# Kernel tuning notes

Measured on AMD Instinct MI355X. Metric: run time of the kernel, lower is better.

The kernel has to match this reference:

```python
import jax, jax.numpy as jnp
import numpy as np
import math

BLOCK_SIZE = 128  # config.block_size


def setup_inputs() -> dict:
    key = jax.random.key(0)
    k1, k2, k3 = jax.random.split(key, 3)
    B, H, S, D = 2, 12, 4096, 64
    return {
        "query_layer": jax.random.normal(k1, (B, H, S, D), dtype=jnp.float32),
        "key_layer": jax.random.normal(k2, (B, H, S, D), dtype=jnp.float32),
        "value_layer": jax.random.normal(k3, (B, H, S, D), dtype=jnp.float32),
        "attention_mask": jnp.zeros((B, 1, 1, S), dtype=jnp.float32),
    }


def reference(query_layer, key_layer, value_layer, attention_mask):
    d = query_layer.shape[-1]
    # [B,H,S,S] attention scores
    scores = jnp.einsum("bhqd,bhkd->bhqk", query_layer, key_layer) / math.sqrt(d)
    scores = scores + attention_mask
    # Faithful to source: the bottom-right block is OVERWRITTEN with
    # tril(ones, -1).T * finfo.min  (0 on/below diag, min strictly above)
    bs = BLOCK_SIZE
    causal_mask = jnp.tril(jnp.ones((bs, bs), dtype=scores.dtype), k=-1).T
    causal_mask = causal_mask * jnp.finfo(scores.dtype).min
    scores = scores.at[..., -bs:, -bs:].set(causal_mask)
    probs = jax.nn.softmax(scores, axis=-1)
    # dropout is identity in eval mode
    return jnp.einsum("bhqk,bhkd->bhqd", probs, value_layer)
```

## Files before the change

### kernel.cpp

```cpp
#include <hip/hip_runtime.h>

#define S_LEN 4096
#define DH    64
#define BQ    128
#define BK    64
#define NTILE (S_LEN / BK)
#define QBLKS (S_LEN / BQ)
#define NBH   24
#define NHEADS 12

#define BQ2   64
#define BK2   32
#define NT2   (S_LEN / BK2)
#define QB2   (S_LEN / BQ2)

typedef __attribute__((ext_vector_type(8))) short short8;
typedef __attribute__((ext_vector_type(4))) short short4v;
typedef __attribute__((ext_vector_type(4))) float f32x4;
typedef __attribute__((ext_vector_type(4))) unsigned uint4v;

#define KSTR 72
#define VSTR 72
#define LOG2E 1.44269504088896f
#define MCONST (-12.99718425f)

#define NKCH (NBH * S_LEN * DH / 8)

__device__ __forceinline__ short f2bf(float x) {
    unsigned u = __builtin_bit_cast(unsigned, x);
    return (short)((u + 0x8000u) >> 16);
}

typedef __attribute__((address_space(1))) const unsigned int guint;
typedef __attribute__((address_space(3))) unsigned int luint;
__device__ __forceinline__ void g2l16(const short* g, short* l) {
    __builtin_amdgcn_global_load_lds((guint*)g, (luint*)l, 16, 0, 0);
}

__device__ __forceinline__ void swap32(unsigned &a, unsigned &b) {
    asm("v_permlane32_swap_b32 %0, %1" : "+v"(a), "+v"(b));
}
__device__ __forceinline__ void swap16(unsigned &a, unsigned &b) {
    asm("v_permlane16_swap_b32 %0, %1" : "+v"(a), "+v"(b));
}

__global__ __launch_bounds__(256)
void prepass(const float* __restrict__ K, const float* __restrict__ V,
             const float* __restrict__ M, short* __restrict__ Kf,
             short* __restrict__ Vtf, float* __restrict__ Mf)
{
    __shared__ __align__(16) short K_lds[BK * KSTR];
    __shared__ __align__(16) short Vt_lds[DH * VSTR];

    const int tid = threadIdx.x;
    const int bh  = blockIdx.x >> 6;
    const int t   = blockIdx.x & 63;
    const size_t base = ((size_t)bh * S_LEN + (size_t)t * BK) * DH;

    #pragma unroll
    for (int it = 0; it < 4; ++it) {
        int idx = tid + 256 * it;
        int row = idx >> 4, c4 = idx & 15;
        float4 v = *(const float4*)(K + base + (size_t)row * DH + 4 * c4);
        short4v b4 = { f2bf(v.x), f2bf(v.y), f2bf(v.z), f2bf(v.w) };
        *(short4v*)&K_lds[row * KSTR + 4 * c4] = b4;
    }
    {
        int kb = tid >> 4, db = tid & 15;
        const float* vp = V + base + (size_t)(4 * kb) * DH + 4 * db;
        float4 r0 = *(const float4*)(vp);
        float4 r1 = *(const float4*)(vp + DH);
        float4 r2 = *(const float4*)(vp + 2 * DH);
        float4 r3 = *(const float4*)(vp + 3 * DH);
        short4v c0 = { f2bf(r0.x), f2bf(r1.x), f2bf(r2.x), f2bf(r3.x) };
        short4v c1 = { f2bf(r0.y), f2bf(r1.y), f2bf(r2.y), f2bf(r3.y) };
        short4v c2 = { f2bf(r0.z), f2bf(r1.z), f2bf(r2.z), f2bf(r3.z) };
        short4v c3 = { f2bf(r0.w), f2bf(r1.w), f2bf(r2.w), f2bf(r3.w) };
        *(short4v*)&Vt_lds[(4 * db + 0) * VSTR + 4 * kb] = c0;
        *(short4v*)&Vt_lds[(4 * db + 1) * VSTR + 4 * kb] = c1;
        *(short4v*)&Vt_lds[(4 * db + 2) * VSTR + 4 * kb] = c2;
        *(short4v*)&Vt_lds[(4 * db + 3) * VSTR + 4 * kb] = c3;
    }
    __syncthreads();

    const size_t obase = (size_t)(bh * NTILE + t) * 4096;
    #pragma unroll
    for (int e = 0; e < 2; ++e) {
        int ci = tid + 256 * e;
        int lane = ci & 63, n = lane & 15, q = lane >> 4;
        {
            int kt = (ci >> 6) & 1, mt = ci >> 7;
            short8 f = *(const short8*)&K_lds[(16 * mt + n) * KSTR + 32 * kt + 8 * q];
            *(short8*)&Kf[obase + (size_t)ci * 8] = f;
        }
        {
            int d = (ci >> 6) & 3, kt2 = (ci >> 8) & 1;
            short8 g2 = *(const short8*)&Vt_lds[(16 * d + n) * VSTR + 32 * kt2 + 8 * q];
            *(short8*)&Vtf[obase + (size_t)ci * 8] = g2;
        }
    }
    if ((bh % NHEADS) == 0 && tid < 16) {
        int b_idx = bh / NHEADS;
        float4 mv = *(const float4*)(M + (size_t)b_idx * S_LEN + t * BK + 4 * tid);
        mv.x = mv.x * LOG2E + MCONST;
        mv.y = mv.y * LOG2E + MCONST;
        mv.z = mv.z * LOG2E + MCONST;
        mv.w = mv.w * LOG2E + MCONST;
        *(float4*)&Mf[(size_t)b_idx * S_LEN + t * BK + 4 * tid] = mv;
    }
}

__global__ __launch_bounds__(128, 8)
void fa9(const float* __restrict__ Q, const short* __restrict__ Kf,
         const short* __restrict__ Vtf, const float* __restrict__ Mf,
         float* __restrict__ O)
{
    __shared__ __align__(16) short Ks[2][2048];
    __shared__ __align__(16) short Vs[2][2048];

    const int tid  = threadIdx.x;
    const int w    = tid >> 6;
    const int lane = tid & 63;
    const int n    = lane & 15;
    const int quad = lane >> 4;

    const int bid  = blockIdx.x;
    const int x    = bid & 7;
    const int g    = bid >> 3;
    const int bh   = x + 8 * (g >> 6);
    const int qblk = g & 63;
    const bool special = (qblk >= QB2 - 2);

    const size_t base  = (size_t)bh * S_LEN * DH;
    const int    b_idx = bh / NHEADS;

    const float QSCALE = 0.125f * LOG2E;
    const int qbase = qblk * BQ2 + w * 32;
    short8 qf[2][2];
    #pragma unroll
    for (int s = 0; s < 2; ++s) {
        const float* qp = Q + base + (size_t)(qbase + 16 * s + n) * DH;
        #pragma unroll
        for (int kt = 0; kt < 2; ++kt) {
            const float* p = qp + 32 * kt + 8 * quad;
            float4 a = *(const float4*)p;
            float4 b = *(const float4*)(p + 4);
            short8 f;
            f[0] = f2bf(a.x * QSCALE); f[1] = f2bf(a.y * QSCALE);
            f[2] = f2bf(a.z * QSCALE); f[3] = f2bf(a.w * QSCALE);
            f[4] = f2bf(b.x * QSCALE); f[5] = f2bf(b.y * QSCALE);
            f[6] = f2bf(b.z * QSCALE); f[7] = f2bf(b.w * QSCALE);
            qf[s][kt] = f;
        }
    }

    f32x4 o[4][2];
    #pragma unroll
    for (int d = 0; d < 4; ++d)
        #pragma unroll
        for (int s = 0; s < 2; ++s) o[d][s] = (f32x4){0.f, 0.f, 0.f, 0.f};
    f32x4 lsum[2] = { (f32x4){0.f,0.f,0.f,0.f}, (f32x4){0.f,0.f,0.f,0.f} };

    const short8 ONES = { 0x3F80, 0x3F80, 0x3F80, 0x3F80,
                          0x3F80, 0x3F80, 0x3F80, 0x3F80 };
    const float* mrow = Mf + (size_t)b_idx * S_LEN;
    const short* Kg = Kf  + (size_t)(bh * NTILE) * 4096;
    const short* Vg = Vtf + (size_t)(bh * NTILE) * 4096;

    #pragma unroll
    for (int i = 0; i < 2; ++i) {
        int c = 2 * w + i;
        g2l16(Kg + c * 512 + lane * 8, &Ks[0][c * 512]);
        g2l16(Vg + c * 512 + lane * 8, &Vs[0][c * 512]);
    }
    __syncthreads();

    for (int t = 0; t < NT2; ++t) {
        const bool sp = special && t >= NT2 - 4;
        const int  cur = t & 1, nxt = cur ^ 1;

        if (t + 1 < NT2) {
            const short* kg = Kg + (size_t)(t + 1) * 2048;
            const short* vg = Vg + (size_t)(t + 1) * 2048;
            #pragma unroll
            for (int i = 0; i < 2; ++i) {
                int c = 2 * w + i;
                g2l16(kg + c * 512 + lane * 8, &Ks[nxt][c * 512]);
                g2l16(vg + c * 512 + lane * 8, &Vs[nxt][c * 512]);
            }
        }

        short8 pf[2];
        if (!sp) {
            unsigned u[2][2][2];
            #pragma unroll
            for (int m = 0; m < 2; ++m) {
                short8 k0 = *(const short8*)&Ks[cur][(2 * m    ) * 512 + lane * 8];
                short8 k1 = *(const short8*)&Ks[cur][(2 * m + 1) * 512 + lane * 8];
                f32x4 mk = *(const f32x4*)(mrow + t * BK2 + 16 * m + 4 * quad);
                #pragma unroll
                for (int s = 0; s < 2; ++s) {
                    f32x4 c = mk;
                    c = __builtin_amdgcn_mfma_f32_16x16x32_bf16(k0, qf[s][0], c, 0, 0, 0);
                    c = __builtin_amdgcn_mfma_f32_16x16x32_bf16(k1, qf[s][1], c, 0, 0, 0);
                    float p0 = __builtin_amdgcn_exp2f(c[0]);
                    float p1 = __builtin_amdgcn_exp2f(c[1]);
                    float p2 = __builtin_amdgcn_exp2f(c[2]);
                    float p3 = __builtin_amdgcn_exp2f(c[3]);
                    unsigned d0 = __builtin_amdgcn_perm(
                        __builtin_bit_cast(unsigned, p1),
                        __builtin_bit_cast(unsigned, p0), 0x07060302u);
                    unsigned d1 = __builtin_amdgcn_perm(
                        __builtin_bit_cast(unsigned, p3),
                        __builtin_bit_cast(unsigned, p2), 0x07060302u);
                    u[m][s][0] = d0;
                    u[m][s][1] = d1;
                }
            }
            #pragma unroll
            for (int s = 0; s < 2; ++s) {
                unsigned X0 = u[0][s][0], Y0 = u[1][s][0];
                unsigned X1 = u[0][s][1], Y1 = u[1][s][1];
                swap32(X0, Y0); swap16(X0, Y0);
                swap32(X1, Y1); swap16(X1, Y1);
                uint4v pc = (uint4v){X0, X1, Y0, Y1};
                pf[s] = __builtin_bit_cast(short8, pc);
            }
        } else {
            #pragma unroll
            for (int s = 0; s < 2; ++s) {
                const int qs = qbase + 16 * s + n;
                const int kb = BK2 * t + 8 * quad;
                unsigned c0 = (kb     <= qs ? 0x3900u : 0u) | (kb + 1 <= qs ? 0x39000000u : 0u);
                unsigned c1 = (kb + 2 <= qs ? 0x3900u : 0u) | (kb + 3 <= qs ? 0x39000000u : 0u);
                unsigned c2 = (kb + 4 <= qs ? 0x3900u : 0u) | (kb + 5 <= qs ? 0x39000000u : 0u);
                unsigned c3 = (kb + 6 <= qs ? 0x3900u : 0u) | (kb + 7 <= qs ? 0x39000000u : 0u);
                uint4v pc = (uint4v){c0, c1, c2, c3};
                pf[s] = __builtin_bit_cast(short8, pc);
            }
        }

        lsum[0] = __builtin_amdgcn_mfma_f32_16x16x32_bf16(ONES, pf[0], lsum[0], 0, 0, 0);
        lsum[1] = __builtin_amdgcn_mfma_f32_16x16x32_bf16(ONES, pf[1], lsum[1], 0, 0, 0);

        #pragma unroll
        for (int d = 0; d < 4; ++d) {
            short8 vf = *(const short8*)&Vs[cur][d * 512 + lane * 8];
            o[d][0] = __builtin_amdgcn_mfma_f32_16x16x32_bf16(vf, pf[0], o[d][0], 0, 0, 0);
            o[d][1] = __builtin_amdgcn_mfma_f32_16x16x32_bf16(vf, pf[1], o[d][1], 0, 0, 0);
        }

        __syncthreads();
    }

    #pragma unroll
    for (int s = 0; s < 2; ++s) {
        float inv = 1.0f / lsum[s][0];
        float* op = O + base + (size_t)(qbase + 16 * s + n) * DH;
        #pragma unroll
        for (int d = 0; d < 4; ++d) {
            f32x4 r = o[d][s] * inv;
            *(f32x4*)(op + 16 * d + 4 * quad) = r;
        }
    }
}

extern "C" void kernel_launch(void* const* d_in, const int* in_sizes, int n_in,
                              void* d_out, int out_size, void* d_ws, size_t ws_size,
                              hipStream_t stream) {
    const float* Q = (const float*)d_in[0];
    const float* K = (const float*)d_in[1];
    const float* V = (const float*)d_in[2];
    const float* M = (const float*)d_in[3];
    float* O = (float*)d_out;

    short* Kf  = (short*)d_ws;
    short* Vtf = Kf + (size_t)NKCH * 8;
    float* Mf  = (float*)(Vtf + (size_t)NKCH * 8);

    prepass<<<dim3(NBH * NTILE), dim3(256), 0, stream>>>(K, V, M, Kf, Vtf, Mf);
    fa9<<<dim3(NBH * QB2), dim3(128), 0, stream>>>(Q, Kf, Vtf, Mf, O);
}
```

Measured before the change: 257.9 us.

## Enlarge attention tiles to 128 queries by 64 keys with four-wave blocks

The attention kernel moves from 2-wave blocks covering 64 query rows and 32-key tiles to 4-wave blocks covering 128 query rows and 64-key tiles. Each 64-key tile is processed as two 32-key halves inside the same stage. Each staged K/V tile is now shared by twice as many query rows, which halves the K/V traffic from global memory and L2 and halves the number of barriers per key. In exchange, LDS per block doubles, launch bounds allow fewer resident waves per CU, and the grid has half as many blocks.

After: 230.0 us. 10.8% less time.

```diff
diff --git a/kernel.cpp b/kernel.cpp
--- a/kernel.cpp
+++ b/kernel.cpp
@@ -8,11 +8,6 @@
 #define QBLKS (S_LEN / BQ)
 #define NBH   24
 #define NHEADS 12
-
-#define BQ2   64
-#define BK2   32
-#define NT2   (S_LEN / BK2)
-#define QB2   (S_LEN / BQ2)
 
 typedef __attribute__((ext_vector_type(8))) short short8;
 typedef __attribute__((ext_vector_type(4))) short short4v;
@@ -110,13 +105,13 @@
     }
 }
 
-__global__ __launch_bounds__(128, 8)
-void fa9(const float* __restrict__ Q, const short* __restrict__ Kf,
-         const short* __restrict__ Vtf, const float* __restrict__ Mf,
-         float* __restrict__ O)
+__global__ __launch_bounds__(256, 3)
+void fa10(const float* __restrict__ Q, const short* __restrict__ Kf,
+          const short* __restrict__ Vtf, const float* __restrict__ Mf,
+          float* __restrict__ O)
 {
-    __shared__ __align__(16) short Ks[2][2048];
-    __shared__ __align__(16) short Vs[2][2048];
+    __shared__ __align__(16) short Ks[2][4096];
+    __shared__ __align__(16) short Vs[2][4096];
 
     const int tid  = threadIdx.x;
     const int w    = tid >> 6;
@@ -127,19 +122,19 @@
     const int bid  = blockIdx.x;
     const int x    = bid & 7;
     const int g    = bid >> 3;
-    const int bh   = x + 8 * (g >> 6);
-    const int qblk = g & 63;
-    const bool special = (qblk >= QB2 - 2);
+    const int bh   = x + 8 * (g >> 5);
+    const int qblk = g & 31;
+    const bool special = (qblk == QBLKS - 1);
 
     const size_t base  = (size_t)bh * S_LEN * DH;
     const int    b_idx = bh / NHEADS;
 
     const float QSCALE = 0.125f * LOG2E;
-    const int qbase = qblk * BQ2 + w * 32;
+    const int q0 = qblk * BQ + w * 32;
     short8 qf[2][2];
     #pragma unroll
     for (int s = 0; s < 2; ++s) {
-        const float* qp = Q + base + (size_t)(qbase + 16 * s + n) * DH;
+        const float* qp = Q + base + (size_t)(q0 + 16 * s + n) * DH;
         #pragma unroll
         for (int kt = 0; kt < 2; ++kt) {
             const float* p = qp + 32 * kt + 8 * quad;
@@ -175,13 +170,13 @@
     }
     __syncthreads();
 
-    for (int t = 0; t < NT2; ++t) {
-        const bool sp = special && t >= NT2 - 4;
+    for (int t = 0; t < NTILE; ++t) {
+        const bool sp = special && t >= NTILE - 2;
         const int  cur = t & 1, nxt = cur ^ 1;
 
-        if (t + 1 < NT2) {
-            const short* kg = Kg + (size_t)(t + 1) * 2048;
-            const short* vg = Vg + (size_t)(t + 1) * 2048;
+        if (t + 1 < NTILE) {
+            const short* kg = Kg + (size_t)(t + 1) * 4096;
+            const short* vg = Vg + (size_t)(t + 1) * 4096;
             #pragma unroll
             for (int i = 0; i < 2; ++i) {
                 int c = 2 * w + i;
@@ -190,64 +185,68 @@
             }
         }
 
-        short8 pf[2];
-        if (!sp) {
-            unsigned u[2][2][2];
-            #pragma unroll
-            for (int m = 0; m < 2; ++m) {
-                short8 k0 = *(const short8*)&Ks[cur][(2 * m    ) * 512 + lane * 8];
-                short8 k1 = *(const short8*)&Ks[cur][(2 * m + 1) * 512 + lane * 8];
-                f32x4 mk = *(const f32x4*)(mrow + t * BK2 + 16 * m + 4 * quad);
+        #pragma unroll
+        for (int h = 0; h < 2; ++h) {
+            short8 pf[2];
+            if (!sp) {
+                unsigned u[2][2][2];
+                #pragma unroll
+                for (int mm = 0; mm < 2; ++mm) {
+                    const int mt = 2 * h + mm;
+                    short8 k0 = *(const short8*)&Ks[cur][(2 * mt    ) * 512 + lane * 8];
+                    short8 k1 = *(const short8*)&Ks[cur][(2 * mt + 1) * 512 + lane * 8];
+                    f32x4 mk = *(const f32x4*)(mrow + t * BK + 16 * mt + 4 * quad);
+                    #pragma unroll
+                    for (int s = 0; s < 2; ++s) {
+                        f32x4 c = mk;
+                        c = __builtin_amdgcn_mfma_f32_16x16x32_bf16(k0, qf[s][0], c, 0, 0, 0);
+                        c = __builtin_amdgcn_mfma_f32_16x16x32_bf16(k1, qf[s][1], c, 0, 0, 0);
+                        float p0 = __builtin_amdgcn_exp2f(c[0]);
+                        float p1 = __builtin_amdgcn_exp2f(c[1]);
+                        float p2 = __builtin_amdgcn_exp2f(c[2]);
+                        float p3 = __builtin_amdgcn_exp2f(c[3]);
+                        unsigned d0 = __builtin_amdgcn_perm(
+                            __builtin_bit_cast(unsigned, p1),
+                            __builtin_bit_cast(unsigned, p0), 0x07060302u);
+                        unsigned d1 = __builtin_amdgcn_perm(
+                            __builtin_bit_cast(unsigned, p3),
+                            __builtin_bit_cast(unsigned, p2), 0x07060302u);
+                        u[mm][s][0] = d0;
+                        u[mm][s][1] = d1;
+                    }
+                }
                 #pragma unroll
                 for (int s = 0; s < 2; ++s) {
-                    f32x4 c = mk;
-                    c = __builtin_amdgcn_mfma_f32_16x16x32_bf16(k0, qf[s][0], c, 0, 0, 0);
-                    c = __builtin_amdgcn_mfma_f32_16x16x32_bf16(k1, qf[s][1], c, 0, 0, 0);
-                    float p0 = __builtin_amdgcn_exp2f(c[0]);
-                    float p1 = __builtin_amdgcn_exp2f(c[1]);
-                    float p2 = __builtin_amdgcn_exp2f(c[2]);
-                    float p3 = __builtin_amdgcn_exp2f(c[3]);
-                    unsigned d0 = __builtin_amdgcn_perm(
-                        __builtin_bit_cast(unsigned, p1),
-                        __builtin_bit_cast(unsigned, p0), 0x07060302u);
-                    unsigned d1 = __builtin_amdgcn_perm(
-                        __builtin_bit_cast(unsigned, p3),
-                        __builtin_bit_cast(unsigned, p2), 0x07060302u);
-                    u[m][s][0] = d0;
-                    u[m][s][1] = d1;
+                    unsigned X0 = u[0][s][0], Y0 = u[1][s][0];
+                    unsigned X1 = u[0][s][1], Y1 = u[1][s][1];
+                    swap32(X0, Y0); swap16(X0, Y0);
+                    swap32(X1, Y1); swap16(X1, Y1);
+                    uint4v pc = (uint4v){X0, X1, Y0, Y1};
+                    pf[s] = __builtin_bit_cast(short8, pc);
+                }
+            } else {
+                #pragma unroll
+                for (int s = 0; s < 2; ++s) {
+                    const int qs = q0 + 16 * s + n;
+                    const int kb = BK * t + 32 * h + 8 * quad;
+                    unsigned c0 = (kb     <= qs ? 0x3900u : 0u) | (kb + 1 <= qs ? 0x39000000u : 0u);
+                    unsigned c1 = (kb + 2 <= qs ? 0x3900u : 0u) | (kb + 3 <= qs ? 0x39000000u : 0u);
+                    unsigned c2 = (kb + 4 <= qs ? 0x3900u : 0u) | (kb + 5 <= qs ? 0x39000000u : 0u);
+                    unsigned c3 = (kb + 6 <= qs ? 0x3900u : 0u) | (kb + 7 <= qs ? 0x39000000u : 0u);
+                    uint4v pc = (uint4v){c0, c1, c2, c3};
+                    pf[s] = __builtin_bit_cast(short8, pc);
                 }
             }
+
+            lsum[0] = __builtin_amdgcn_mfma_f32_16x16x32_bf16(ONES, pf[0], lsum[0], 0, 0, 0);
+            lsum[1] = __builtin_amdgcn_mfma_f32_16x16x32_bf16(ONES, pf[1], lsum[1], 0, 0, 0);
+
             #pragma unroll
-            for (int s = 0; s < 2; ++s) {
-                unsigned X0 = u[0][s][0], Y0 = u[1][s][0];
-                unsigned X1 = u[0][s][1], Y1 = u[1][s][1];
-                swap32(X0, Y0); swap16(X0, Y0);
-                swap32(X1, Y1); swap16(X1, Y1);
-                uint4v pc = (uint4v){X0, X1, Y0, Y1};
-                pf[s] = __builtin_bit_cast(short8, pc);
+            for (int d = 0; d < 4; ++d) {
+                short8 vf = *(const short8*)&Vs[cur][(h * 4 + d) * 512 + lane * 8];
+                o[d][0] = __builtin_amdgcn_mfma_f32_16x16x32_bf16(vf, pf[0], o[d][0], 0, 0, 0);
+                o[d][1] = __builtin_amdgcn_mfma_f32_16x16x32_bf16(vf, pf[1], o[d][1], 0, 0, 0);
             }
-        } else {
-            #pragma unroll
-            for (int s = 0; s < 2; ++s) {
-                const int qs = qbase + 16 * s + n;
-                const int kb = BK2 * t + 8 * quad;
-                unsigned c0 = (kb     <= qs ? 0x3900u : 0u) | (kb + 1 <= qs ? 0x39000000u : 0u);
-                unsigned c1 = (kb + 2 <= qs ? 0x3900u : 0u) | (kb + 3 <= qs ? 0x39000000u : 0u);
-                unsigned c2 = (kb + 4 <= qs ? 0x3900u : 0u) | (kb + 5 <= qs ? 0x39000000u : 0u);
-                unsigned c3 = (kb + 6 <= qs ? 0x3900u : 0u) | (kb + 7 <= qs ? 0x39000000u : 0u);
-                uint4v pc = (uint4v){c0, c1, c2, c3};
-                pf[s] = __builtin_bit_cast(short8, pc);
-            }
-        }
-
-        lsum[0] = __builtin_amdgcn_mfma_f32_16x16x32_bf16(ONES, pf[0], lsum[0], 0, 0, 0);
-        lsum[1] = __builtin_amdgcn_mfma_f32_16x16x32_bf16(ONES, pf[1], lsum[1], 0, 0, 0);
-
-        #pragma unroll
-        for (int d = 0; d < 4; ++d) {
-            short8 vf = *(const short8*)&Vs[cur][d * 512 + lane * 8];
-            o[d][0] = __builtin_amdgcn_mfma_f32_16x16x32_bf16(vf, pf[0], o[d][0], 0, 0, 0);
-            o[d][1] = __builtin_amdgcn_mfma_f32_16x16x32_bf16(vf, pf[1], o[d][1], 0, 0, 0);
         }
 
         __syncthreads();
@@ -256,7 +255,8 @@
     #pragma unroll
     for (int s = 0; s < 2; ++s) {
         float inv = 1.0f / lsum[s][0];
-        float* op = O + base + (size_t)(qbase + 16 * s + n) * DH;
+        int qg = q0 + 16 * s + n;
+        float* op = O + base + (size_t)qg * DH;
         #pragma unroll
         for (int d = 0; d < 4; ++d) {
             f32x4 r = o[d][s] * inv;
@@ -279,5 +279,5 @@
     float* Mf  = (float*)(Vtf + (size_t)NKCH * 8);
 
     prepass<<<dim3(NBH * NTILE), dim3(256), 0, stream>>>(K, V, M, Kf, Vtf, Mf);
-    fa9<<<dim3(NBH * QB2), dim3(128), 0, stream>>>(Q, Kf, Vtf, Mf, O);
-}
+    fa10<<<dim3(NBH * QBLKS), dim3(256), 0, stream>>>(Q, Kf, Vtf, Mf, O);
+}
```
